# Optimization experiments

Hardware: AMD Instinct MI355X
Metric: run time of the kernel (lower is better)

Reference implementation:

```python
import jax, jax.numpy as jnp
import numpy as np

B, V, J, H, W = 32, 2, 17, 128, 128
TEMP = 0.05   # SoftArgmax2D softmax_temp
EPS = 1e-12


def _soft_argmax(hm):
    # hm: (B*V, J, H, W) -> homogeneous coords (B*V, 3, J), per-joint max value
    bv, j, h, w = hm.shape
    p = jax.nn.softmax(hm.reshape(bv, j, h * w) / TEMP, axis=-1).reshape(bv, j, h, w)
    xs = jnp.arange(w, dtype=hm.dtype)
    ys = jnp.arange(h, dtype=hm.dtype)
    x = jnp.einsum('bjhw,w->bj', p, xs)
    y = jnp.einsum('bjhw,h->bj', p, ys)
    coords = jnp.stack([x, y, jnp.ones_like(x)], axis=1)  # (bv, 3, j)
    maxv = hm.max(axis=(-2, -1))
    return coords, maxv


def _skew(t):
    # t: (..., 3) -> skew-symmetric (..., 3, 3), matches -t_mat^T + t_mat in source
    tx, ty, tz = t[..., 0], t[..., 1], t[..., 2]
    z = jnp.zeros_like(tx)
    return jnp.stack([jnp.stack([z, -tz, ty], -1),
                      jnp.stack([tz, z, -tx], -1),
                      jnp.stack([-ty, tx, z], -1)], -2)


def _forward(origin_hms, AP_K, AP_T, LAT_K, LAT_T):
    K = jnp.stack([AP_K, LAT_K], axis=1)              # (B,V,3,3)
    T = jnp.stack([AP_T, LAT_T], axis=1)              # (B,V,4,4)
    R = T[:, :, :3, :3]
    t_std = T[:, :, :3, 3]                            # (B,V,3) standard_cam_T

    # fundamental matrices for all ordered pairs: cam1 = view j, cam2 = view i
    r = jnp.einsum('bimk,bjnk->bijmn', R, R)          # R_i @ R_j^T
    t = t_std[:, :, None, :] - jnp.einsum('bijmn,bjn->bijm', r, t_std)
    M = jnp.einsum('bijmn,bijnk->bijmk', _skew(t), r)
    invK = jnp.linalg.inv(K)
    # F = invK_i^T @ [t]x @ r @ invK_j
    F = jnp.einsum('bipm,bijpq,bjql->bijml', invK, M, invK)  # (B,V,V,3,3)

    coords, maxv = _soft_argmax(origin_hms)           # (B*V,3,J), (B*V,J)
    inv_aff = jnp.diag(jnp.asarray([4.0, 4.0, 1.0], dtype=origin_hms.dtype))  # inverse of 0.25 scale
    img = jnp.einsum('mn,bvnj->bvmj', inv_aff, coords.reshape(B, V, 3, J))
    confi = maxv.reshape(B, V, J)

    # epipolar distances, fully vectorized over (b, i, j) pairs
    l = jnp.einsum('bijmn,bjnk->bijmk', F, img)       # epipolar lines in view i from joints of view j
    cv = img[:, :, None]                              # (B,V,1,3,J)
    num = jnp.sum(cv * l, axis=3) ** 2                # (B,V,V,J)
    lp = jnp.einsum('bijnm,bink->bijmk', F, img)      # F^T @ cv_joints
    div = l[..., 0, :] ** 2 + l[..., 1, :] ** 2 + lp[..., 0, :] ** 2 + lp[..., 1, :] ** 2
    dist_full = jnp.sqrt(num / (div + EPS))           # (B,V,V,J)

    others = np.asarray([[j for j in range(V) if j != i] for i in range(V)])  # (V,V-1)
    ii = np.repeat(np.arange(V)[:, None], V - 1, axis=1)
    distances = dist_full[:, ii, others]              # (B,V,V-1,J)

    # stand-in for ViewWeightNet: confidence minus mean epipolar error, softmax over views
    score = confi - distances.mean(axis=2)            # (B,V,J)
    vw = jax.nn.softmax(score, axis=1)                # (B,V,J)

    mv = jnp.where(maxv > 0.01, maxv, 1e6).reshape(B * V, J, 1, 1)
    hms_norm = origin_hms / mv
    hm4 = hms_norm.reshape(B, V, J, H, W)

    # cat order: self heatmap first, then other views (matches get_warp_weight / cat_hm layout)
    order = np.asarray([[i] + [j for j in range(V) if j != i] for i in range(V)])  # (V,V)
    cat_hm = hm4[:, order]                            # (B,V,V,J,H,W); identity-warp stand-in for CamFusionModule
    ww = vw[:, order]                                 # (B,V,V,J) warp weights
    fused_hm = jnp.sum(ww[..., None, None] * cat_hm, axis=2).reshape(B * V, J, H, W)

    coords2, _ = _soft_argmax(fused_hm)
    img2 = jnp.einsum('mn,bvnj->bvmj', inv_aff, coords2.reshape(B, V, 3, J))
    return img2[:, :, :2, :], fused_hm


def setup_inputs() -> dict:
    key = jax.random.key(0)
    k1, k2, k3, k4, k5 = jax.random.split(key, 5)
    hms = jax.random.uniform(k1, (B * V, J, H, W), dtype=jnp.float32)

    def make_K(k):
        f = 1000.0 + jax.random.normal(k, (B,)) * 10.0
        Km = jnp.zeros((B, 3, 3), dtype=jnp.float32)
        Km = Km.at[:, 0, 0].set(f).at[:, 1, 1].set(f)
        Km = Km.at[:, 0, 2].set(256.0).at[:, 1, 2].set(256.0).at[:, 2, 2].set(1.0)
        return Km

    def make_T(k):
        A = jax.random.normal(k, (B, 3, 3))
        Q, _ = jnp.linalg.qr(A)
        Q = Q * jnp.linalg.det(Q)[:, None, None]  # force det = +1 (proper rotation)
        t = jax.random.normal(jax.random.fold_in(k, 1), (B, 3, 1)) * 0.1 + jnp.asarray([0.0, 0.0, 5.0]).reshape(3, 1)
        bottom = jnp.tile(jnp.asarray([[[0.0, 0.0, 0.0, 1.0]]]), (B, 1, 1))
        return jnp.concatenate([jnp.concatenate([Q, t], axis=2), bottom], axis=1).astype(jnp.float32)

    return {"origin_hms": hms, "AP_K": make_K(k2), "AP_T": make_T(k3),
            "LAT_K": make_K(k4), "LAT_T": make_T(k5)}


def reference(origin_hms, AP_K, AP_T, LAT_K, LAT_T):
    return _forward(origin_hms, AP_K, AP_T, LAT_K, LAT_T)
```

## Files before the change

kernel.cpp:

```cpp
#include <hip/hip_runtime.h>
#include <math.h>

#define NB 32
#define NV 2
#define NJ 17
#define NH 128
#define NW 128
#define MAPN (NH * NW)
#define MAPN4 (MAPN / 4)
#define NMAPS (NB * NV * NJ)
#define NBJ (NB * NJ)
#define OUT0N (NB * NV * 2 * NJ)
#define INV_TEMP 20.0f
#define EPS_D 1e-12f

typedef float vfloat4 __attribute__((ext_vector_type(4)));

__device__ __forceinline__ float waveMax(float v) {
#pragma unroll
    for (int off = 32; off > 0; off >>= 1)
        v = fmaxf(v, __shfl_xor(v, off, 64));
    return v;
}
__device__ __forceinline__ float waveSum(float v) {
#pragma unroll
    for (int off = 32; off > 0; off >>= 1)
        v += __shfl_xor(v, off, 64);
    return v;
}

__global__ __launch_bounds__(512) void k_stats(const float* __restrict__ hms,
                                               float* __restrict__ maxv,
                                               float* __restrict__ cx,
                                               float* __restrict__ cy) {
    const int map = blockIdx.x;
    const int tid = threadIdx.x;
    const float4* src = (const float4*)hms + (size_t)map * MAPN4;

    float mx = -3.402823466e38f;
    float s = 0.f, sx = 0.f, sy = 0.f;
#pragma unroll
    for (int u = 0; u < 8; ++u) {
        const int i4 = tid + u * 512;
        const float4 v = src[i4];
        mx = fmaxf(mx, fmaxf(fmaxf(v.x, v.y), fmaxf(v.z, v.w)));
        const int e0 = i4 * 4;
        const float hh = (float)(e0 >> 7);
        const float ww = (float)(e0 & 127);
        const float ea = __expf((v.x - 1.0f) * INV_TEMP);
        const float eb = __expf((v.y - 1.0f) * INV_TEMP);
        const float ec = __expf((v.z - 1.0f) * INV_TEMP);
        const float ed = __expf((v.w - 1.0f) * INV_TEMP);
        const float se = (ea + eb) + (ec + ed);
        s += se;
        sy += se * hh;
        sx += ea * ww + eb * (ww + 1.f) + ec * (ww + 2.f) + ed * (ww + 3.f);
    }

    __shared__ float rM[8], rS[8], rX[8], rY[8];
    const int wid = tid >> 6, lane = tid & 63;
    mx = waveMax(mx);
    s = waveSum(s); sx = waveSum(sx); sy = waveSum(sy);
    if (lane == 0) { rM[wid] = mx; rS[wid] = s; rX[wid] = sx; rY[wid] = sy; }
    __syncthreads();
    if (tid == 0) {
        float M = rM[0], S = rS[0], SX = rX[0], SY = rY[0];
#pragma unroll
        for (int w = 1; w < 8; ++w) {
            M = fmaxf(M, rM[w]); S += rS[w]; SX += rX[w]; SY += rY[w];
        }
        maxv[map] = M;
        cx[map] = SX / S;
        cy[map] = SY / S;
    }
}

__device__ __forceinline__ void inv3(const float K[3][3], float o[3][3]) {
    const float a = K[0][0], b = K[0][1], c = K[0][2];
    const float d = K[1][0], e = K[1][1], f = K[1][2];
    const float g = K[2][0], h = K[2][1], i = K[2][2];
    const float A =  (e * i - f * h);
    const float Bv = -(d * i - f * g);
    const float C =  (d * h - e * g);
    const float det = a * A + b * Bv + c * C;
    const float id = 1.0f / det;
    o[0][0] = A * id;                 o[0][1] = -(b * i - c * h) * id;  o[0][2] = (b * f - c * e) * id;
    o[1][0] = Bv * id;                o[1][1] = (a * i - c * g) * id;   o[1][2] = -(a * f - c * d) * id;
    o[2][0] = C * id;                 o[2][1] = -(a * h - b * g) * id;  o[2][2] = (a * e - b * d) * id;
}

__global__ void k_weights(const float* __restrict__ APK, const float* __restrict__ APT,
                          const float* __restrict__ LATK, const float* __restrict__ LATT,
                          const float* __restrict__ maxv, const float* __restrict__ cx,
                          const float* __restrict__ cy, float* __restrict__ wgt) {
    const int t = blockIdx.x * blockDim.x + threadIdx.x;
    if (t >= NBJ) return;
    const int b = t / NJ, k = t % NJ;

    float Km[2][3][3], R[2][3][3], tr[2][3], iK[2][3][3];
    for (int r = 0; r < 3; ++r)
        for (int c = 0; c < 3; ++c) {
            Km[0][r][c] = APK[b * 9 + r * 3 + c];
            Km[1][r][c] = LATK[b * 9 + r * 3 + c];
            R[0][r][c] = APT[b * 16 + r * 4 + c];
            R[1][r][c] = LATT[b * 16 + r * 4 + c];
        }
    for (int r = 0; r < 3; ++r) {
        tr[0][r] = APT[b * 16 + r * 4 + 3];
        tr[1][r] = LATT[b * 16 + r * 4 + 3];
    }
    inv3(Km[0], iK[0]);
    inv3(Km[1], iK[1]);

    float F[2][3][3];
    for (int i = 0; i < 2; ++i) {
        const int j = 1 - i;
        float r[3][3];
        for (int m = 0; m < 3; ++m)
            for (int n = 0; n < 3; ++n)
                r[m][n] = R[i][m][0] * R[j][n][0] + R[i][m][1] * R[j][n][1] + R[i][m][2] * R[j][n][2];
        float tv[3];
        for (int m = 0; m < 3; ++m)
            tv[m] = tr[i][m] - (r[m][0] * tr[j][0] + r[m][1] * tr[j][1] + r[m][2] * tr[j][2]);
        const float S[3][3] = {{0.f, -tv[2], tv[1]}, {tv[2], 0.f, -tv[0]}, {-tv[1], tv[0], 0.f}};
        float M[3][3];
        for (int m = 0; m < 3; ++m)
            for (int n = 0; n < 3; ++n)
                M[m][n] = S[m][0] * r[0][n] + S[m][1] * r[1][n] + S[m][2] * r[2][n];
        float tmp[3][3];
        for (int p = 0; p < 3; ++p)
            for (int l = 0; l < 3; ++l)
                tmp[p][l] = M[p][0] * iK[j][0][l] + M[p][1] * iK[j][1][l] + M[p][2] * iK[j][2][l];
        for (int m = 0; m < 3; ++m)
            for (int l = 0; l < 3; ++l)
                F[i][m][l] = iK[i][0][m] * tmp[0][l] + iK[i][1][m] * tmp[1][l] + iK[i][2][m] * tmp[2][l];
    }

    float img[2][3], conf[2];
    for (int i = 0; i < 2; ++i) {
        const int idx = (b * 2 + i) * NJ + k;
        img[i][0] = 4.0f * cx[idx];
        img[i][1] = 4.0f * cy[idx];
        img[i][2] = 1.0f;
        conf[i] = maxv[idx];
    }

    float score[2];
    for (int i = 0; i < 2; ++i) {
        const int j = 1 - i;
        const float l0 = F[i][0][0] * img[j][0] + F[i][0][1] * img[j][1] + F[i][0][2] * img[j][2];
        const float l1 = F[i][1][0] * img[j][0] + F[i][1][1] * img[j][1] + F[i][1][2] * img[j][2];
        const float l2 = F[i][2][0] * img[j][0] + F[i][2][1] * img[j][1] + F[i][2][2] * img[j][2];
        const float sdot = img[i][0] * l0 + img[i][1] * l1 + img[i][2] * l2;
        const float num = sdot * sdot;
        const float lp0 = F[i][0][0] * img[i][0] + F[i][1][0] * img[i][1] + F[i][2][0] * img[i][2];
        const float lp1 = F[i][0][1] * img[i][0] + F[i][1][1] * img[i][1] + F[i][2][1] * img[i][2];
        const float dv = l0 * l0 + l1 * l1 + lp0 * lp0 + lp1 * lp1;
        score[i] = conf[i] - sqrtf(num / (dv + EPS_D));
    }

    const float mS = fmaxf(score[0], score[1]);
    const float e0 = __expf(score[0] - mS), e1 = __expf(score[1] - mS);
    const float inv = 1.0f / (e0 + e1);
    const float vw[2] = {e0 * inv, e1 * inv};
    for (int i = 0; i < 2; ++i) {
        const int idx = (b * 2 + i) * NJ + k;
        const float mv = conf[i] > 0.01f ? conf[i] : 1e6f;
        wgt[idx] = vw[i] / mv;
    }
}

__global__ __launch_bounds__(512) void k_fuse(const float* __restrict__ hms,
                                              const float* __restrict__ wgt,
                                              float* __restrict__ out) {
    const int blk = blockIdx.x;
    const int b = blk / NJ, j = blk % NJ;
    const int tid = threadIdx.x;

    const size_t m0 = ((size_t)(b * 2 + 0) * NJ + j) * MAPN4;
    const size_t m1 = ((size_t)(b * 2 + 1) * NJ + j) * MAPN4;
    const float4* A = (const float4*)hms + m0;
    const float4* Cm = (const float4*)hms + m1;
    float* outhm = out + OUT0N;
    vfloat4* O0 = reinterpret_cast<vfloat4*>(outhm) + m0;
    vfloat4* O1 = reinterpret_cast<vfloat4*>(outhm) + m1;
    const float w0 = wgt[(b * 2 + 0) * NJ + j];
    const float w1 = wgt[(b * 2 + 1) * NJ + j];

    float s = 0.f, sx = 0.f, sy = 0.f;
#pragma unroll
    for (int u = 0; u < 8; ++u) {
        const int i4 = tid + u * 512;
        const float4 a = A[i4];
        const float4 c = Cm[i4];
        vfloat4 f;
        f.x = w0 * a.x + w1 * c.x;
        f.y = w0 * a.y + w1 * c.y;
        f.z = w0 * a.z + w1 * c.z;
        f.w = w0 * a.w + w1 * c.w;
        __builtin_nontemporal_store(f, &O0[i4]);
        __builtin_nontemporal_store(f, &O1[i4]);
        const int e0 = i4 * 4;
        const float hh = (float)(e0 >> 7);
        const float ww = (float)(e0 & 127);
        const float ea = __expf((f.x - 1.0f) * INV_TEMP);
        const float eb = __expf((f.y - 1.0f) * INV_TEMP);
        const float ec = __expf((f.z - 1.0f) * INV_TEMP);
        const float ed = __expf((f.w - 1.0f) * INV_TEMP);
        const float se = (ea + eb) + (ec + ed);
        s += se;
        sy += se * hh;
        sx += ea * ww + eb * (ww + 1.f) + ec * (ww + 2.f) + ed * (ww + 3.f);
    }

    __shared__ float rS[8], rX[8], rY[8];
    const int wid = tid >> 6, lane = tid & 63;
    s = waveSum(s); sx = waveSum(sx); sy = waveSum(sy);
    if (lane == 0) { rS[wid] = s; rX[wid] = sx; rY[wid] = sy; }
    __syncthreads();
    if (tid == 0) {
        float S = rS[0], SX = rX[0], SY = rY[0];
#pragma unroll
        for (int w = 1; w < 8; ++w) { S += rS[w]; SX += rX[w]; SY += rY[w]; }
        const float x4 = 4.0f * (SX / S);
        const float y4 = 4.0f * (SY / S);
        out[((b * 2 + 0) * 2 + 0) * NJ + j] = x4;
        out[((b * 2 + 0) * 2 + 1) * NJ + j] = y4;
        out[((b * 2 + 1) * 2 + 0) * NJ + j] = x4;
        out[((b * 2 + 1) * 2 + 1) * NJ + j] = y4;
    }
}

extern "C" void kernel_launch(void* const* d_in, const int* in_sizes, int n_in,
                              void* d_out, int out_size, void* d_ws, size_t ws_size,
                              hipStream_t stream) {
    const float* hms  = (const float*)d_in[0];
    const float* APK  = (const float*)d_in[1];
    const float* APT  = (const float*)d_in[2];
    const float* LATK = (const float*)d_in[3];
    const float* LATT = (const float*)d_in[4];
    float* out = (float*)d_out;
    float* ws  = (float*)d_ws;

    float* maxv = ws;
    float* cx   = ws + NMAPS;
    float* cy   = ws + 2 * NMAPS;
    float* wgt  = ws + 3 * NMAPS;

    k_stats<<<NMAPS, 512, 0, stream>>>(hms, maxv, cx, cy);
    k_weights<<<(NBJ + 63) / 64, 64, 0, stream>>>(APK, APT, LATK, LATT, maxv, cx, cy, wgt);
    k_fuse<<<NBJ, 512, 0, stream>>>(hms, wgt, out);
}
```

Before: 142.4 us.

## Fuse stats, weight and fuse kernels into one register-resident kernel

The three kernels (per-map soft-argmax stats, per-joint epipolar weights, weighted fusion) are merged into one kernel with one block per (batch, joint). Both views' heatmaps are loaded once into registers (16 float4 per thread) and reused for the stats pass and the fusion pass, so the second global read of the input and two launches go away. In exchange, only 544 blocks run instead of 1088 for the stats phase, register pressure rises, and a single thread computes the weights while the rest of the block waits.

```diff
diff --git a/kernel.cpp b/kernel.cpp
--- a/kernel.cpp
+++ b/kernel.cpp
@@ -29,52 +29,6 @@
     return v;
 }
 
-__global__ __launch_bounds__(512) void k_stats(const float* __restrict__ hms,
-                                               float* __restrict__ maxv,
-                                               float* __restrict__ cx,
-                                               float* __restrict__ cy) {
-    const int map = blockIdx.x;
-    const int tid = threadIdx.x;
-    const float4* src = (const float4*)hms + (size_t)map * MAPN4;
-
-    float mx = -3.402823466e38f;
-    float s = 0.f, sx = 0.f, sy = 0.f;
-#pragma unroll
-    for (int u = 0; u < 8; ++u) {
-        const int i4 = tid + u * 512;
-        const float4 v = src[i4];
-        mx = fmaxf(mx, fmaxf(fmaxf(v.x, v.y), fmaxf(v.z, v.w)));
-        const int e0 = i4 * 4;
-        const float hh = (float)(e0 >> 7);
-        const float ww = (float)(e0 & 127);
-        const float ea = __expf((v.x - 1.0f) * INV_TEMP);
-        const float eb = __expf((v.y - 1.0f) * INV_TEMP);
-        const float ec = __expf((v.z - 1.0f) * INV_TEMP);
-        const float ed = __expf((v.w - 1.0f) * INV_TEMP);
-        const float se = (ea + eb) + (ec + ed);
-        s += se;
-        sy += se * hh;
-        sx += ea * ww + eb * (ww + 1.f) + ec * (ww + 2.f) + ed * (ww + 3.f);
-    }
-
-    __shared__ float rM[8], rS[8], rX[8], rY[8];
-    const int wid = tid >> 6, lane = tid & 63;
-    mx = waveMax(mx);
-    s = waveSum(s); sx = waveSum(sx); sy = waveSum(sy);
-    if (lane == 0) { rM[wid] = mx; rS[wid] = s; rX[wid] = sx; rY[wid] = sy; }
-    __syncthreads();
-    if (tid == 0) {
-        float M = rM[0], S = rS[0], SX = rX[0], SY = rY[0];
-#pragma unroll
-        for (int w = 1; w < 8; ++w) {
-            M = fmaxf(M, rM[w]); S += rS[w]; SX += rX[w]; SY += rY[w];
-        }
-        maxv[map] = M;
-        cx[map] = SX / S;
-        cy[map] = SY / S;
-    }
-}
-
 __device__ __forceinline__ void inv3(const float K[3][3], float o[3][3]) {
     const float a = K[0][0], b = K[0][1], c = K[0][2];
     const float d = K[1][0], e = K[1][1], f = K[1][2];
@@ -84,115 +38,165 @@
     const float C =  (d * h - e * g);
     const float det = a * A + b * Bv + c * C;
     const float id = 1.0f / det;
-    o[0][0] = A * id;                 o[0][1] = -(b * i - c * h) * id;  o[0][2] = (b * f - c * e) * id;
-    o[1][0] = Bv * id;                o[1][1] = (a * i - c * g) * id;   o[1][2] = -(a * f - c * d) * id;
-    o[2][0] = C * id;                 o[2][1] = -(a * h - b * g) * id;  o[2][2] = (a * e - b * d) * id;
-}
-
-__global__ void k_weights(const float* __restrict__ APK, const float* __restrict__ APT,
-                          const float* __restrict__ LATK, const float* __restrict__ LATT,
-                          const float* __restrict__ maxv, const float* __restrict__ cx,
-                          const float* __restrict__ cy, float* __restrict__ wgt) {
-    const int t = blockIdx.x * blockDim.x + threadIdx.x;
-    if (t >= NBJ) return;
-    const int b = t / NJ, k = t % NJ;
-
-    float Km[2][3][3], R[2][3][3], tr[2][3], iK[2][3][3];
-    for (int r = 0; r < 3; ++r)
-        for (int c = 0; c < 3; ++c) {
-            Km[0][r][c] = APK[b * 9 + r * 3 + c];
-            Km[1][r][c] = LATK[b * 9 + r * 3 + c];
-            R[0][r][c] = APT[b * 16 + r * 4 + c];
-            R[1][r][c] = LATT[b * 16 + r * 4 + c];
-        }
-    for (int r = 0; r < 3; ++r) {
-        tr[0][r] = APT[b * 16 + r * 4 + 3];
-        tr[1][r] = LATT[b * 16 + r * 4 + 3];
-    }
-    inv3(Km[0], iK[0]);
-    inv3(Km[1], iK[1]);
-
-    float F[2][3][3];
-    for (int i = 0; i < 2; ++i) {
-        const int j = 1 - i;
-        float r[3][3];
-        for (int m = 0; m < 3; ++m)
-            for (int n = 0; n < 3; ++n)
-                r[m][n] = R[i][m][0] * R[j][n][0] + R[i][m][1] * R[j][n][1] + R[i][m][2] * R[j][n][2];
-        float tv[3];
-        for (int m = 0; m < 3; ++m)
-            tv[m] = tr[i][m] - (r[m][0] * tr[j][0] + r[m][1] * tr[j][1] + r[m][2] * tr[j][2]);
-        const float S[3][3] = {{0.f, -tv[2], tv[1]}, {tv[2], 0.f, -tv[0]}, {-tv[1], tv[0], 0.f}};
-        float M[3][3];
-        for (int m = 0; m < 3; ++m)
-            for (int n = 0; n < 3; ++n)
-                M[m][n] = S[m][0] * r[0][n] + S[m][1] * r[1][n] + S[m][2] * r[2][n];
-        float tmp[3][3];
-        for (int p = 0; p < 3; ++p)
-            for (int l = 0; l < 3; ++l)
-                tmp[p][l] = M[p][0] * iK[j][0][l] + M[p][1] * iK[j][1][l] + M[p][2] * iK[j][2][l];
-        for (int m = 0; m < 3; ++m)
-            for (int l = 0; l < 3; ++l)
-                F[i][m][l] = iK[i][0][m] * tmp[0][l] + iK[i][1][m] * tmp[1][l] + iK[i][2][m] * tmp[2][l];
-    }
-
-    float img[2][3], conf[2];
-    for (int i = 0; i < 2; ++i) {
-        const int idx = (b * 2 + i) * NJ + k;
-        img[i][0] = 4.0f * cx[idx];
-        img[i][1] = 4.0f * cy[idx];
-        img[i][2] = 1.0f;
-        conf[i] = maxv[idx];
-    }
-
-    float score[2];
-    for (int i = 0; i < 2; ++i) {
-        const int j = 1 - i;
-        const float l0 = F[i][0][0] * img[j][0] + F[i][0][1] * img[j][1] + F[i][0][2] * img[j][2];
-        const float l1 = F[i][1][0] * img[j][0] + F[i][1][1] * img[j][1] + F[i][1][2] * img[j][2];
-        const float l2 = F[i][2][0] * img[j][0] + F[i][2][1] * img[j][1] + F[i][2][2] * img[j][2];
-        const float sdot = img[i][0] * l0 + img[i][1] * l1 + img[i][2] * l2;
-        const float num = sdot * sdot;
-        const float lp0 = F[i][0][0] * img[i][0] + F[i][1][0] * img[i][1] + F[i][2][0] * img[i][2];
-        const float lp1 = F[i][0][1] * img[i][0] + F[i][1][1] * img[i][1] + F[i][2][1] * img[i][2];
-        const float dv = l0 * l0 + l1 * l1 + lp0 * lp0 + lp1 * lp1;
-        score[i] = conf[i] - sqrtf(num / (dv + EPS_D));
-    }
-
-    const float mS = fmaxf(score[0], score[1]);
-    const float e0 = __expf(score[0] - mS), e1 = __expf(score[1] - mS);
-    const float inv = 1.0f / (e0 + e1);
-    const float vw[2] = {e0 * inv, e1 * inv};
-    for (int i = 0; i < 2; ++i) {
-        const int idx = (b * 2 + i) * NJ + k;
-        const float mv = conf[i] > 0.01f ? conf[i] : 1e6f;
-        wgt[idx] = vw[i] / mv;
-    }
-}
-
-__global__ __launch_bounds__(512) void k_fuse(const float* __restrict__ hms,
-                                              const float* __restrict__ wgt,
-                                              float* __restrict__ out) {
+    o[0][0] = A * id;  o[0][1] = -(b * i - c * h) * id;  o[0][2] = (b * f - c * e) * id;
+    o[1][0] = Bv * id; o[1][1] = (a * i - c * g) * id;   o[1][2] = -(a * f - c * d) * id;
+    o[2][0] = C * id;  o[2][1] = -(a * h - b * g) * id;  o[2][2] = (a * e - b * d) * id;
+}
+
+__global__ __launch_bounds__(512, 4) void k_all(const float* __restrict__ hms,
+                                                const float* __restrict__ APK,
+                                                const float* __restrict__ APT,
+                                                const float* __restrict__ LATK,
+                                                const float* __restrict__ LATT,
+                                                float* __restrict__ out) {
     const int blk = blockIdx.x;
     const int b = blk / NJ, j = blk % NJ;
     const int tid = threadIdx.x;
+    const int wid = tid >> 6, lane = tid & 63;
 
     const size_t m0 = ((size_t)(b * 2 + 0) * NJ + j) * MAPN4;
     const size_t m1 = ((size_t)(b * 2 + 1) * NJ + j) * MAPN4;
-    const float4* A = (const float4*)hms + m0;
-    const float4* Cm = (const float4*)hms + m1;
+    const float4* A  = (const float4*)hms + m0;
+    const float4* Bm = (const float4*)hms + m1;
+
+    float4 va[8], vb[8];
+#pragma unroll
+    for (int u = 0; u < 8; ++u) {
+        va[u] = A[tid + u * 512];
+        vb[u] = Bm[tid + u * 512];
+    }
+
+    float mx0 = -1e30f, mx1 = -1e30f;
+    float s0 = 0.f, sx0 = 0.f, sy0 = 0.f;
+    float s1 = 0.f, sx1 = 0.f, sy1 = 0.f;
+#pragma unroll
+    for (int u = 0; u < 8; ++u) {
+        const int e0 = (tid + u * 512) * 4;
+        const float hh = (float)(e0 >> 7);
+        const float ww = (float)(e0 & 127);
+        {
+            const float4 v = va[u];
+            mx0 = fmaxf(mx0, fmaxf(fmaxf(v.x, v.y), fmaxf(v.z, v.w)));
+            const float ea = __expf((v.x - 1.0f) * INV_TEMP);
+            const float eb = __expf((v.y - 1.0f) * INV_TEMP);
+            const float ec = __expf((v.z - 1.0f) * INV_TEMP);
+            const float ed = __expf((v.w - 1.0f) * INV_TEMP);
+            const float se = (ea + eb) + (ec + ed);
+            s0 += se; sy0 += se * hh;
+            sx0 += ea * ww + eb * (ww + 1.f) + ec * (ww + 2.f) + ed * (ww + 3.f);
+        }
+        {
+            const float4 v = vb[u];
+            mx1 = fmaxf(mx1, fmaxf(fmaxf(v.x, v.y), fmaxf(v.z, v.w)));
+            const float ea = __expf((v.x - 1.0f) * INV_TEMP);
+            const float eb = __expf((v.y - 1.0f) * INV_TEMP);
+            const float ec = __expf((v.z - 1.0f) * INV_TEMP);
+            const float ed = __expf((v.w - 1.0f) * INV_TEMP);
+            const float se = (ea + eb) + (ec + ed);
+            s1 += se; sy1 += se * hh;
+            sx1 += ea * ww + eb * (ww + 1.f) + ec * (ww + 2.f) + ed * (ww + 3.f);
+        }
+    }
+
+    __shared__ float red[8][8];
+    __shared__ float wsh[2];
+    mx0 = waveMax(mx0); mx1 = waveMax(mx1);
+    s0 = waveSum(s0); sx0 = waveSum(sx0); sy0 = waveSum(sy0);
+    s1 = waveSum(s1); sx1 = waveSum(sx1); sy1 = waveSum(sy1);
+    if (lane == 0) {
+        red[0][wid] = mx0; red[1][wid] = s0; red[2][wid] = sx0; red[3][wid] = sy0;
+        red[4][wid] = mx1; red[5][wid] = s1; red[6][wid] = sx1; red[7][wid] = sy1;
+    }
+    __syncthreads();
+
+    if (tid == 0) {
+        float M0 = red[0][0], S0 = red[1][0], SX0 = red[2][0], SY0 = red[3][0];
+        float M1 = red[4][0], S1 = red[5][0], SX1 = red[6][0], SY1 = red[7][0];
+#pragma unroll
+        for (int w = 1; w < 8; ++w) {
+            M0 = fmaxf(M0, red[0][w]); S0 += red[1][w]; SX0 += red[2][w]; SY0 += red[3][w];
+            M1 = fmaxf(M1, red[4][w]); S1 += red[5][w]; SX1 += red[6][w]; SY1 += red[7][w];
+        }
+        const float conf[2] = {M0, M1};
+        float img[2][3];
+        img[0][0] = 4.0f * (SX0 / S0); img[0][1] = 4.0f * (SY0 / S0); img[0][2] = 1.0f;
+        img[1][0] = 4.0f * (SX1 / S1); img[1][1] = 4.0f * (SY1 / S1); img[1][2] = 1.0f;
+
+        float Km[2][3][3], R[2][3][3], tr[2][3], iK[2][3][3];
+        for (int r = 0; r < 3; ++r)
+            for (int c = 0; c < 3; ++c) {
+                Km[0][r][c] = APK[b * 9 + r * 3 + c];
+                Km[1][r][c] = LATK[b * 9 + r * 3 + c];
+                R[0][r][c] = APT[b * 16 + r * 4 + c];
+                R[1][r][c] = LATT[b * 16 + r * 4 + c];
+            }
+        for (int r = 0; r < 3; ++r) {
+            tr[0][r] = APT[b * 16 + r * 4 + 3];
+            tr[1][r] = LATT[b * 16 + r * 4 + 3];
+        }
+        inv3(Km[0], iK[0]);
+        inv3(Km[1], iK[1]);
+
+        float F[2][3][3];
+        for (int i = 0; i < 2; ++i) {
+            const int jj = 1 - i;
+            float r[3][3];
+            for (int m = 0; m < 3; ++m)
+                for (int n = 0; n < 3; ++n)
+                    r[m][n] = R[i][m][0] * R[jj][n][0] + R[i][m][1] * R[jj][n][1] + R[i][m][2] * R[jj][n][2];
+            float tv[3];
+            for (int m = 0; m < 3; ++m)
+                tv[m] = tr[i][m] - (r[m][0] * tr[jj][0] + r[m][1] * tr[jj][1] + r[m][2] * tr[jj][2]);
+            const float S[3][3] = {{0.f, -tv[2], tv[1]}, {tv[2], 0.f, -tv[0]}, {-tv[1], tv[0], 0.f}};
+            float M[3][3];
+            for (int m = 0; m < 3; ++m)
+                for (int n = 0; n < 3; ++n)
+                    M[m][n] = S[m][0] * r[0][n] + S[m][1] * r[1][n] + S[m][2] * r[2][n];
+            float tmp[3][3];
+            for (int p = 0; p < 3; ++p)
+                for (int l = 0; l < 3; ++l)
+                    tmp[p][l] = M[p][0] * iK[jj][0][l] + M[p][1] * iK[jj][1][l] + M[p][2] * iK[jj][2][l];
+            for (int m = 0; m < 3; ++m)
+                for (int l = 0; l < 3; ++l)
+                    F[i][m][l] = iK[i][0][m] * tmp[0][l] + iK[i][1][m] * tmp[1][l] + iK[i][2][m] * tmp[2][l];
+        }
+
+        float score[2];
+        for (int i = 0; i < 2; ++i) {
+            const int jj = 1 - i;
+            const float l0 = F[i][0][0] * img[jj][0] + F[i][0][1] * img[jj][1] + F[i][0][2] * img[jj][2];
+            const float l1 = F[i][1][0] * img[jj][0] + F[i][1][1] * img[jj][1] + F[i][1][2] * img[jj][2];
+            const float l2 = F[i][2][0] * img[jj][0] + F[i][2][1] * img[jj][1] + F[i][2][2] * img[jj][2];
+            const float sdot = img[i][0] * l0 + img[i][1] * l1 + img[i][2] * l2;
+            const float num = sdot * sdot;
+            const float lp0 = F[i][0][0] * img[i][0] + F[i][1][0] * img[i][1] + F[i][2][0] * img[i][2];
+            const float lp1 = F[i][0][1] * img[i][0] + F[i][1][1] * img[i][1] + F[i][2][1] * img[i][2];
+            const float dv = l0 * l0 + l1 * l1 + lp0 * lp0 + lp1 * lp1;
+            score[i] = conf[i] - sqrtf(num / (dv + EPS_D));
+        }
+
+        const float mS = fmaxf(score[0], score[1]);
+        const float e0 = __expf(score[0] - mS), e1 = __expf(score[1] - mS);
+        const float inv = 1.0f / (e0 + e1);
+        const float mv0 = conf[0] > 0.01f ? conf[0] : 1e6f;
+        const float mv1 = conf[1] > 0.01f ? conf[1] : 1e6f;
+        wsh[0] = (e0 * inv) / mv0;
+        wsh[1] = (e1 * inv) / mv1;
+    }
+    __syncthreads();
+    const float w0 = wsh[0];
+    const float w1 = wsh[1];
+
     float* outhm = out + OUT0N;
     vfloat4* O0 = reinterpret_cast<vfloat4*>(outhm) + m0;
     vfloat4* O1 = reinterpret_cast<vfloat4*>(outhm) + m1;
-    const float w0 = wgt[(b * 2 + 0) * NJ + j];
-    const float w1 = wgt[(b * 2 + 1) * NJ + j];
 
     float s = 0.f, sx = 0.f, sy = 0.f;
 #pragma unroll
     for (int u = 0; u < 8; ++u) {
         const int i4 = tid + u * 512;
-        const float4 a = A[i4];
-        const float4 c = Cm[i4];
+        const float4 a = va[u];
+        const float4 c = vb[u];
         vfloat4 f;
         f.x = w0 * a.x + w1 * c.x;
         f.y = w0 * a.y + w1 * c.y;
@@ -208,20 +212,17 @@
         const float ec = __expf((f.z - 1.0f) * INV_TEMP);
         const float ed = __expf((f.w - 1.0f) * INV_TEMP);
         const float se = (ea + eb) + (ec + ed);
-        s += se;
-        sy += se * hh;
+        s += se; sy += se * hh;
         sx += ea * ww + eb * (ww + 1.f) + ec * (ww + 2.f) + ed * (ww + 3.f);
     }
 
-    __shared__ float rS[8], rX[8], rY[8];
-    const int wid = tid >> 6, lane = tid & 63;
     s = waveSum(s); sx = waveSum(sx); sy = waveSum(sy);
-    if (lane == 0) { rS[wid] = s; rX[wid] = sx; rY[wid] = sy; }
+    if (lane == 0) { red[0][wid] = s; red[1][wid] = sx; red[2][wid] = sy; }
     __syncthreads();
     if (tid == 0) {
-        float S = rS[0], SX = rX[0], SY = rY[0];
-#pragma unroll
-        for (int w = 1; w < 8; ++w) { S += rS[w]; SX += rX[w]; SY += rY[w]; }
+        float S = red[0][0], SX = red[1][0], SY = red[2][0];
+#pragma unroll
+        for (int w = 1; w < 8; ++w) { S += red[0][w]; SX += red[1][w]; SY += red[2][w]; }
         const float x4 = 4.0f * (SX / S);
         const float y4 = 4.0f * (SY / S);
         out[((b * 2 + 0) * 2 + 0) * NJ + j] = x4;
@@ -240,14 +241,6 @@
     const float* LATK = (const float*)d_in[3];
     const float* LATT = (const float*)d_in[4];
     float* out = (float*)d_out;
-    float* ws  = (float*)d_ws;
-
-    float* maxv = ws;
-    float* cx   = ws + NMAPS;
-    float* cy   = ws + 2 * NMAPS;
-    float* wgt  = ws + 3 * NMAPS;
-
-    k_stats<<<NMAPS, 512, 0, stream>>>(hms, maxv, cx, cy);
-    k_weights<<<(NBJ + 63) / 64, 64, 0, stream>>>(APK, APT, LATK, LATT, maxv, cx, cy, wgt);
-    k_fuse<<<NBJ, 512, 0, stream>>>(hms, wgt, out);
-}
+
+    k_all<<<NBJ, 512, 0, stream>>>(hms, APK, APT, LATK, LATT, out);
+}
```

Measured after the change: 141.7 us. No clear change (-0.5%).

## Split fuse kernel into per-map chunks with atomic accumulation and final kernel

Applied to the files above, without the earlier changes.

The fuse stage now runs each (batch, joint) map as 8 blocks of 256 threads instead of one block of 512, which gives 4352 blocks rather than 544 and so better occupancy and memory parallelism. Partial softmax sums are combined with global atomicAdd into accumulators that the weights kernel zeroes. A new small kernel computes the final coordinates from those sums. This adds one kernel launch and atomic traffic, and float atomics make the summation order nondeterministic.

```diff
diff --git a/kernel.cpp b/kernel.cpp
--- a/kernel.cpp
+++ b/kernel.cpp
@@ -13,6 +13,8 @@
 #define OUT0N (NB * NV * 2 * NJ)
 #define INV_TEMP 20.0f
 #define EPS_D 1e-12f
+#define FUSE_CHUNKS 8
+#define CHUNK4 (MAPN4 / FUSE_CHUNKS)
 
 typedef float vfloat4 __attribute__((ext_vector_type(4)));
 
@@ -37,8 +39,7 @@
     const int tid = threadIdx.x;
     const float4* src = (const float4*)hms + (size_t)map * MAPN4;
 
-    float mx = -3.402823466e38f;
-    float s = 0.f, sx = 0.f, sy = 0.f;
+    float mx = -1e30f, s = 0.f, sx = 0.f, sy = 0.f;
 #pragma unroll
     for (int u = 0; u < 8; ++u) {
         const int i4 = tid + u * 512;
@@ -52,8 +53,7 @@
         const float ec = __expf((v.z - 1.0f) * INV_TEMP);
         const float ed = __expf((v.w - 1.0f) * INV_TEMP);
         const float se = (ea + eb) + (ec + ed);
-        s += se;
-        sy += se * hh;
+        s += se; sy += se * hh;
         sx += ea * ww + eb * (ww + 1.f) + ec * (ww + 2.f) + ed * (ww + 3.f);
     }
 
@@ -84,16 +84,18 @@
     const float C =  (d * h - e * g);
     const float det = a * A + b * Bv + c * C;
     const float id = 1.0f / det;
-    o[0][0] = A * id;                 o[0][1] = -(b * i - c * h) * id;  o[0][2] = (b * f - c * e) * id;
-    o[1][0] = Bv * id;                o[1][1] = (a * i - c * g) * id;   o[1][2] = -(a * f - c * d) * id;
-    o[2][0] = C * id;                 o[2][1] = -(a * h - b * g) * id;  o[2][2] = (a * e - b * d) * id;
+    o[0][0] = A * id;  o[0][1] = -(b * i - c * h) * id;  o[0][2] = (b * f - c * e) * id;
+    o[1][0] = Bv * id; o[1][1] = (a * i - c * g) * id;   o[1][2] = -(a * f - c * d) * id;
+    o[2][0] = C * id;  o[2][1] = -(a * h - b * g) * id;  o[2][2] = (a * e - b * d) * id;
 }
 
 __global__ void k_weights(const float* __restrict__ APK, const float* __restrict__ APT,
                           const float* __restrict__ LATK, const float* __restrict__ LATT,
                           const float* __restrict__ maxv, const float* __restrict__ cx,
-                          const float* __restrict__ cy, float* __restrict__ wgt) {
+                          const float* __restrict__ cy, float* __restrict__ wgt,
+                          float* __restrict__ accAll ) {
     const int t = blockIdx.x * blockDim.x + threadIdx.x;
+    if (t < 3 * NBJ) accAll[t] = 0.0f;
     if (t >= NBJ) return;
     const int b = t / NJ, k = t % NJ;
 
@@ -114,14 +116,14 @@
 
     float F[2][3][3];
     for (int i = 0; i < 2; ++i) {
-        const int j = 1 - i;
+        const int jj = 1 - i;
         float r[3][3];
         for (int m = 0; m < 3; ++m)
             for (int n = 0; n < 3; ++n)
-                r[m][n] = R[i][m][0] * R[j][n][0] + R[i][m][1] * R[j][n][1] + R[i][m][2] * R[j][n][2];
+                r[m][n] = R[i][m][0] * R[jj][n][0] + R[i][m][1] * R[jj][n][1] + R[i][m][2] * R[jj][n][2];
         float tv[3];
         for (int m = 0; m < 3; ++m)
-            tv[m] = tr[i][m] - (r[m][0] * tr[j][0] + r[m][1] * tr[j][1] + r[m][2] * tr[j][2]);
+            tv[m] = tr[i][m] - (r[m][0] * tr[jj][0] + r[m][1] * tr[jj][1] + r[m][2] * tr[jj][2]);
         const float S[3][3] = {{0.f, -tv[2], tv[1]}, {tv[2], 0.f, -tv[0]}, {-tv[1], tv[0], 0.f}};
         float M[3][3];
         for (int m = 0; m < 3; ++m)
@@ -130,7 +132,7 @@
         float tmp[3][3];
         for (int p = 0; p < 3; ++p)
             for (int l = 0; l < 3; ++l)
-                tmp[p][l] = M[p][0] * iK[j][0][l] + M[p][1] * iK[j][1][l] + M[p][2] * iK[j][2][l];
+                tmp[p][l] = M[p][0] * iK[jj][0][l] + M[p][1] * iK[jj][1][l] + M[p][2] * iK[jj][2][l];
         for (int m = 0; m < 3; ++m)
             for (int l = 0; l < 3; ++l)
                 F[i][m][l] = iK[i][0][m] * tmp[0][l] + iK[i][1][m] * tmp[1][l] + iK[i][2][m] * tmp[2][l];
@@ -147,10 +149,10 @@
 
     float score[2];
     for (int i = 0; i < 2; ++i) {
-        const int j = 1 - i;
-        const float l0 = F[i][0][0] * img[j][0] + F[i][0][1] * img[j][1] + F[i][0][2] * img[j][2];
-        const float l1 = F[i][1][0] * img[j][0] + F[i][1][1] * img[j][1] + F[i][1][2] * img[j][2];
-        const float l2 = F[i][2][0] * img[j][0] + F[i][2][1] * img[j][1] + F[i][2][2] * img[j][2];
+        const int jj = 1 - i;
+        const float l0 = F[i][0][0] * img[jj][0] + F[i][0][1] * img[jj][1] + F[i][0][2] * img[jj][2];
+        const float l1 = F[i][1][0] * img[jj][0] + F[i][1][1] * img[jj][1] + F[i][1][2] * img[jj][2];
+        const float l2 = F[i][2][0] * img[jj][0] + F[i][2][1] * img[jj][1] + F[i][2][2] * img[jj][2];
         const float sdot = img[i][0] * l0 + img[i][1] * l1 + img[i][2] * l2;
         const float num = sdot * sdot;
         const float lp0 = F[i][0][0] * img[i][0] + F[i][1][0] * img[i][1] + F[i][2][0] * img[i][2];
@@ -162,25 +164,28 @@
     const float mS = fmaxf(score[0], score[1]);
     const float e0 = __expf(score[0] - mS), e1 = __expf(score[1] - mS);
     const float inv = 1.0f / (e0 + e1);
-    const float vw[2] = {e0 * inv, e1 * inv};
-    for (int i = 0; i < 2; ++i) {
-        const int idx = (b * 2 + i) * NJ + k;
-        const float mv = conf[i] > 0.01f ? conf[i] : 1e6f;
-        wgt[idx] = vw[i] / mv;
-    }
-}
-
-__global__ __launch_bounds__(512) void k_fuse(const float* __restrict__ hms,
+    const float mv0 = conf[0] > 0.01f ? conf[0] : 1e6f;
+    const float mv1 = conf[1] > 0.01f ? conf[1] : 1e6f;
+    wgt[(b * 2 + 0) * NJ + k] = (e0 * inv) / mv0;
+    wgt[(b * 2 + 1) * NJ + k] = (e1 * inv) / mv1;
+}
+
+__global__ __launch_bounds__(256) void k_fuse(const float* __restrict__ hms,
                                               const float* __restrict__ wgt,
+                                              float* __restrict__ accS,
+                                              float* __restrict__ accX,
+                                              float* __restrict__ accY,
                                               float* __restrict__ out) {
-    const int blk = blockIdx.x;
-    const int b = blk / NJ, j = blk % NJ;
+    const int g = blockIdx.x;
+    const int mapbj = g >> 3;
+    const int chunk = g & (FUSE_CHUNKS - 1);
+    const int b = mapbj / NJ, j = mapbj % NJ;
     const int tid = threadIdx.x;
 
     const size_t m0 = ((size_t)(b * 2 + 0) * NJ + j) * MAPN4;
     const size_t m1 = ((size_t)(b * 2 + 1) * NJ + j) * MAPN4;
-    const float4* A = (const float4*)hms + m0;
-    const float4* Cm = (const float4*)hms + m1;
+    const float4* A  = (const float4*)hms + m0;
+    const float4* Bm = (const float4*)hms + m1;
     float* outhm = out + OUT0N;
     vfloat4* O0 = reinterpret_cast<vfloat4*>(outhm) + m0;
     vfloat4* O1 = reinterpret_cast<vfloat4*>(outhm) + m1;
@@ -189,10 +194,10 @@
 
     float s = 0.f, sx = 0.f, sy = 0.f;
 #pragma unroll
-    for (int u = 0; u < 8; ++u) {
-        const int i4 = tid + u * 512;
+    for (int u = 0; u < 2; ++u) {
+        const int i4 = chunk * CHUNK4 + u * 256 + tid;
         const float4 a = A[i4];
-        const float4 c = Cm[i4];
+        const float4 c = Bm[i4];
         vfloat4 f;
         f.x = w0 * a.x + w1 * c.x;
         f.y = w0 * a.y + w1 * c.y;
@@ -208,27 +213,39 @@
         const float ec = __expf((f.z - 1.0f) * INV_TEMP);
         const float ed = __expf((f.w - 1.0f) * INV_TEMP);
         const float se = (ea + eb) + (ec + ed);
-        s += se;
-        sy += se * hh;
+        s += se; sy += se * hh;
         sx += ea * ww + eb * (ww + 1.f) + ec * (ww + 2.f) + ed * (ww + 3.f);
     }
 
-    __shared__ float rS[8], rX[8], rY[8];
+    __shared__ float rS[4], rX[4], rY[4];
     const int wid = tid >> 6, lane = tid & 63;
     s = waveSum(s); sx = waveSum(sx); sy = waveSum(sy);
     if (lane == 0) { rS[wid] = s; rX[wid] = sx; rY[wid] = sy; }
     __syncthreads();
     if (tid == 0) {
-        float S = rS[0], SX = rX[0], SY = rY[0];
-#pragma unroll
-        for (int w = 1; w < 8; ++w) { S += rS[w]; SX += rX[w]; SY += rY[w]; }
-        const float x4 = 4.0f * (SX / S);
-        const float y4 = 4.0f * (SY / S);
-        out[((b * 2 + 0) * 2 + 0) * NJ + j] = x4;
-        out[((b * 2 + 0) * 2 + 1) * NJ + j] = y4;
-        out[((b * 2 + 1) * 2 + 0) * NJ + j] = x4;
-        out[((b * 2 + 1) * 2 + 1) * NJ + j] = y4;
-    }
+        const float S  = (rS[0] + rS[1]) + (rS[2] + rS[3]);
+        const float SX = (rX[0] + rX[1]) + (rX[2] + rX[3]);
+        const float SY = (rY[0] + rY[1]) + (rY[2] + rY[3]);
+        atomicAdd(&accS[mapbj], S);
+        atomicAdd(&accX[mapbj], SX);
+        atomicAdd(&accY[mapbj], SY);
+    }
+}
+
+__global__ void k_final(const float* __restrict__ accS,
+                        const float* __restrict__ accX,
+                        const float* __restrict__ accY,
+                        float* __restrict__ out) {
+    const int t = blockIdx.x * blockDim.x + threadIdx.x;
+    if (t >= NBJ) return;
+    const int b = t / NJ, j = t % NJ;
+    const float S = accS[t];
+    const float x4 = 4.0f * (accX[t] / S);
+    const float y4 = 4.0f * (accY[t] / S);
+    out[((b * 2 + 0) * 2 + 0) * NJ + j] = x4;
+    out[((b * 2 + 0) * 2 + 1) * NJ + j] = y4;
+    out[((b * 2 + 1) * 2 + 0) * NJ + j] = x4;
+    out[((b * 2 + 1) * 2 + 1) * NJ + j] = y4;
 }
 
 extern "C" void kernel_launch(void* const* d_in, const int* in_sizes, int n_in,
@@ -246,8 +263,13 @@
     float* cx   = ws + NMAPS;
     float* cy   = ws + 2 * NMAPS;
     float* wgt  = ws + 3 * NMAPS;
+    float* accS = ws + 4 * NMAPS;
+    float* accX = accS + NBJ;
+    float* accY = accX + NBJ;
 
     k_stats<<<NMAPS, 512, 0, stream>>>(hms, maxv, cx, cy);
-    k_weights<<<(NBJ + 63) / 64, 64, 0, stream>>>(APK, APT, LATK, LATT, maxv, cx, cy, wgt);
-    k_fuse<<<NBJ, 512, 0, stream>>>(hms, wgt, out);
-}
+    k_weights<<<(3 * NBJ + 255) / 256, 256, 0, stream>>>(APK, APT, LATK, LATT,
+                                                         maxv, cx, cy, wgt, accS);
+    k_fuse<<<NBJ * FUSE_CHUNKS, 256, 0, stream>>>(hms, wgt, accS, accX, accY, out);
+    k_final<<<(NBJ + 255) / 256, 256, 0, stream>>>(accS, accX, accY, out);
+}
```

Result: no change. 143.3 us (+0.7%).
